# Performance work log

Hardware: AMD Instinct MI355X
Metric: run time of the kernel (lower is better)

Reference implementation:

```python
import jax, jax.numpy as jnp
import numpy as np

N, DIM, DK, DV = 8192, 512, 128, 128


def setup_inputs() -> dict:
    key = jax.random.key(0)
    ks = jax.random.split(key, 6)
    s = lambda d: 1.0 / np.sqrt(d)
    return {
        "x": jax.random.normal(ks[0], (N, DIM), jnp.float32),
        "W": jax.random.normal(ks[1], (DK, DIM), jnp.float32) * s(DIM),
        "b": jax.random.normal(ks[2], (DK,), jnp.float32) * s(DIM),
        "Wv": jax.random.normal(ks[3], (DV, DIM), jnp.float32) * s(DIM),
        "bv": jax.random.normal(ks[4], (DV,), jnp.float32) * s(DIM),
        "a": jax.random.normal(ks[5], (2 * DK,), jnp.float32),
    }


def reference(x, W, b, Wv, bv, a):
    dk = a.shape[0] // 2
    wx = x @ W.T + b                      # [n, dk]
    # additive GAT score decomposed into two matvecs + outer sum
    s_src = wx @ a[:dk]                   # [n]
    s_dst = wx @ a[dk:]                   # [n]
    score = s_src[:, None] + s_dst[None, :]  # [n, n]
    score = jax.nn.leaky_relu(score, negative_slope=0.01)
    score = jax.nn.softmax(score, axis=-1)
    v = x @ Wv.T + bv                     # [n, dv]
    return score @ v                      # [n, dv]
```

## Files before the change

### kernel.cpp

```cpp
#include <hip/hip_runtime.h>
#include <math.h>

static constexpr int N    = 8192;
static constexpr int DIM  = 512;
static constexpr int DK   = 128;
static constexpr int DV   = 128;
static constexpr float SLOPE = 0.01f;

static constexpr int NCH  = 256;
static constexpr int CHSZ = 32;
static constexpr int NCOL = 258;

static constexpr int MT  = 128;
static constexpr int BK  = 32;
static constexpr int LDT = 132;

__global__ __launch_bounds__(256) void k_front(const float* __restrict__ x,
                                               const float* __restrict__ W,
                                               const float* __restrict__ b,
                                               const float* __restrict__ a,
                                               float* __restrict__ s_src,
                                               float* __restrict__ s_dst) {
    __shared__ float sa[2 * DK];
    __shared__ float sus[DIM + 32], sud[DIM + 32];
    __shared__ float sc[2];
    int tid = threadIdx.x;
    sa[tid] = a[tid];
    __syncthreads();

    {
        float p = 0.0f;
        if (tid < 64)        p = b[tid] * sa[tid] + b[tid + 64] * sa[tid + 64];
        else if (tid < 128) { int l = tid - 64; p = b[l] * sa[DK + l] + b[l + 64] * sa[DK + 64 + l]; }
#pragma unroll
        for (int off = 32; off > 0; off >>= 1) p += __shfl_down(p, off);
        if (tid == 0)  sc[0] = p;
        if (tid == 64) sc[1] = p;
    }

#pragma unroll
    for (int half = 0; half < 2; ++half) {
        int d = tid + half * 256;
        float us = 0.0f, ud = 0.0f;
#pragma unroll 4
        for (int k = 0; k < DK; ++k) {
            float w = W[(size_t)k * DIM + d];
            us += w * sa[k];
            ud += w * sa[DK + k];
        }
        int dp = d + (d >> 6) * 4;
        sus[dp] = us;
        sud[dp] = ud;
    }
    __syncthreads();

    int r   = tid >> 3;
    int seg = tid & 7;
    int row = blockIdx.x * 32 + r;
    const float* xr = x + (size_t)row * DIM;
    int base  = seg * 64;
    int baseP = base + seg * 4;
    float accs = 0.0f, accd = 0.0f;
#pragma unroll
    for (int i = 0; i < 16; ++i) {
        float4 q  = *reinterpret_cast<const float4*>(xr + base + i * 4);
        float4 u4 = *reinterpret_cast<const float4*>(&sus[baseP + i * 4]);
        float4 w4 = *reinterpret_cast<const float4*>(&sud[baseP + i * 4]);
        accs += q.x * u4.x + q.y * u4.y + q.z * u4.z + q.w * u4.w;
        accd += q.x * w4.x + q.y * w4.y + q.z * w4.z + q.w * w4.w;
    }
#pragma unroll
    for (int off = 4; off > 0; off >>= 1) {
        accs += __shfl_down(accs, off);
        accd += __shfl_down(accd, off);
    }
    if (seg == 0) {
        s_src[row] = accs + sc[0];
        s_dst[row] = accd + sc[1];
    }
}

__global__ __launch_bounds__(256) void k_v(const float* __restrict__ x,
                                           const float* __restrict__ Wv,
                                           float* __restrict__ vpart, int ksplit) {
    __shared__ float At[BK][LDT];
    __shared__ float Bt[BK][LDT];
    int tid = threadIdx.x;
    int mt  = blockIdx.x & 63;
    int ks  = blockIdx.x >> 6;
    int row0 = mt * MT;
    int ksub = DIM / ksplit;
    int kb0  = ks * ksub;
    int nt   = ksub / BK;
    int tx = tid & 15, ty = tid >> 4;

    float acc[8][8];
#pragma unroll
    for (int i = 0; i < 8; ++i)
#pragma unroll
        for (int j = 0; j < 8; ++j) acc[i][j] = 0.0f;

    int fr[4], fk[4];
#pragma unroll
    for (int i = 0; i < 4; ++i) {
        int f = tid + i * 256;
        fr[i] = f >> 3;
        fk[i] = (f & 7) * 4;
    }
    float4 px[4], pw[4];
#pragma unroll
    for (int i = 0; i < 4; ++i) {
        px[i] = *reinterpret_cast<const float4*>(x  + (size_t)(row0 + fr[i]) * DIM + kb0 + fk[i]);
        pw[i] = *reinterpret_cast<const float4*>(Wv + (size_t)fr[i] * DIM + kb0 + fk[i]);
    }

    for (int t = 0; t < nt; ++t) {
#pragma unroll
        for (int i = 0; i < 4; ++i) {
            At[fk[i] + 0][fr[i]] = px[i].x;
            At[fk[i] + 1][fr[i]] = px[i].y;
            At[fk[i] + 2][fr[i]] = px[i].z;
            At[fk[i] + 3][fr[i]] = px[i].w;
            Bt[fk[i] + 0][fr[i]] = pw[i].x;
            Bt[fk[i] + 1][fr[i]] = pw[i].y;
            Bt[fk[i] + 2][fr[i]] = pw[i].z;
            Bt[fk[i] + 3][fr[i]] = pw[i].w;
        }
        __syncthreads();
        if (t < nt - 1) {
            int kb = kb0 + (t + 1) * BK;
#pragma unroll
            for (int i = 0; i < 4; ++i) {
                px[i] = *reinterpret_cast<const float4*>(x  + (size_t)(row0 + fr[i]) * DIM + kb + fk[i]);
                pw[i] = *reinterpret_cast<const float4*>(Wv + (size_t)fr[i] * DIM + kb + fk[i]);
            }
        }
#pragma unroll 4
        for (int kk = 0; kk < BK; ++kk) {
            float4 a0 = *reinterpret_cast<const float4*>(&At[kk][ty * 4]);
            float4 a1 = *reinterpret_cast<const float4*>(&At[kk][64 + ty * 4]);
            float4 b0 = *reinterpret_cast<const float4*>(&Bt[kk][tx * 4]);
            float4 b1 = *reinterpret_cast<const float4*>(&Bt[kk][64 + tx * 4]);
            float av[8] = {a0.x, a0.y, a0.z, a0.w, a1.x, a1.y, a1.z, a1.w};
            float bw[8] = {b0.x, b0.y, b0.z, b0.w, b1.x, b1.y, b1.z, b1.w};
#pragma unroll
            for (int i = 0; i < 8; ++i)
#pragma unroll
                for (int j = 0; j < 8; ++j) acc[i][j] += av[i] * bw[j];
        }
        __syncthreads();
    }

#pragma unroll
    for (int rh = 0; rh < 2; ++rh)
#pragma unroll
        for (int i = 0; i < 4; ++i) {
            int row = row0 + rh * 64 + ty * 4 + i;
            float* dst = vpart + ((size_t)ks * N + row) * DV;
#pragma unroll
            for (int ch = 0; ch < 2; ++ch) {
                float4 o;
                o.x = acc[rh * 4 + i][ch * 4 + 0];
                o.y = acc[rh * 4 + i][ch * 4 + 1];
                o.z = acc[rh * 4 + i][ch * 4 + 2];
                o.w = acc[rh * 4 + i][ch * 4 + 3];
                *reinterpret_cast<float4*>(dst + ch * 64 + tx * 4) = o;
            }
        }
}

__global__ void k_vred(const float* __restrict__ vpart, const float* __restrict__ bv,
                       float* __restrict__ v, int ksplit) {
    int fi = blockIdx.x * 256 + threadIdx.x;
    const float4* vp = reinterpret_cast<const float4*>(vpart);
    float4 s = vp[fi];
    for (int ksp = 1; ksp < ksplit; ++ksp) {
        float4 q = vp[(size_t)ksp * (N * DV / 4) + fi];
        s.x += q.x; s.y += q.y; s.z += q.z; s.w += q.w;
    }
    float4 bb = reinterpret_cast<const float4*>(bv)[fi & 31];
    s.x += bb.x; s.y += bb.y; s.z += bb.z; s.w += bb.w;
    reinterpret_cast<float4*>(v)[fi] = s;
}

__global__ __launch_bounds__(256) void k_rank_scatter(const float* __restrict__ s_dst,
                                                      float* __restrict__ d_sorted,
                                                      int* __restrict__ perm) {
    __shared__ __align__(16) float sd[N];
    __shared__ int part[256];
    int tid = threadIdx.x;
    for (int t = tid; t < N / 4; t += 256)
        reinterpret_cast<float4*>(sd)[t] = reinterpret_cast<const float4*>(s_dst)[t];
    __syncthreads();
    int j0  = blockIdx.x * 16;
    int jj  = tid >> 4;
    int seg = tid & 15;
    int j   = j0 + jj;
    float dj = sd[j];
    int cnt = 0;
    const float4* sdv = reinterpret_cast<const float4*>(sd);
    int cbase = seg * 128;
    for (int c = 0; c < 128; ++c) {
        float4 q = sdv[cbase + c];
        int i0 = (cbase + c) * 4;
        cnt += (q.x < dj || (q.x == dj && (i0 + 0) < j));
        cnt += (q.y < dj || (q.y == dj && (i0 + 1) < j));
        cnt += (q.z < dj || (q.z == dj && (i0 + 2) < j));
        cnt += (q.w < dj || (q.w == dj && (i0 + 3) < j));
    }
    part[tid] = cnt;
    __syncthreads();
    if (tid < 16) {
        int s = 0;
#pragma unroll
        for (int t = 0; t < 16; ++t) s += part[tid * 16 + t];
        int jw = j0 + tid;
        d_sorted[s] = sd[jw];
        perm[s] = jw;
    }
}

__global__ void k_chunk_tot(const float* __restrict__ d_sorted, const int* __restrict__ perm,
                            const float* __restrict__ v, double* __restrict__ chunk_tot) {
    int ch = blockIdx.x, tid = threadIdx.x;
    __shared__ float e1s[CHSZ], e2s[CHSZ];
    __shared__ int pk[CHSZ];
    float dmax = d_sorted[N - 1];
    if (tid < CHSZ) {
        float d = d_sorted[ch * CHSZ + tid];
        e1s[tid] = expf(d - dmax);
        e2s[tid] = expf(SLOPE * d);
        pk[tid]  = perm[ch * CHSZ + tid];
    }
    __syncthreads();
    int col = tid & 127;
    bool isP2 = tid >= 128;
    double acc = 0.0;
    for (int k = 0; k < CHSZ; ++k) {
        float e = isP2 ? e2s[k] : e1s[k];
        acc += (double)e * (double)v[(size_t)pk[k] * DV + col];
    }
    chunk_tot[(size_t)ch * NCOL + tid] = acc;
    if (tid == 0) {
        double z = 0.0;
        for (int k = 0; k < CHSZ; ++k) z += (double)e1s[k];
        chunk_tot[(size_t)ch * NCOL + 256] = z;
    }
    if (tid == 1) {
        double z = 0.0;
        for (int k = 0; k < CHSZ; ++k) z += (double)e2s[k];
        chunk_tot[(size_t)ch * NCOL + 257] = z;
    }
}

__global__ void k_chunk_off(const double* __restrict__ chunk_tot, double* __restrict__ chunk_off,
                            double* __restrict__ totals) {
    __shared__ double s[256];
    int col = blockIdx.x;
    int tid = threadIdx.x;
    double val = chunk_tot[(size_t)tid * NCOL + col];
    s[tid] = val;
    __syncthreads();
    for (int off = 1; off < 256; off <<= 1) {
        double t = (tid >= off) ? s[tid - off] : 0.0;
        __syncthreads();
        s[tid] += t;
        __syncthreads();
    }
    chunk_off[(size_t)tid * NCOL + col] = s[tid] - val;
    if (tid == 255) totals[col] = s[255];
}

__global__ void k_scan(const float* __restrict__ d_sorted, const int* __restrict__ perm,
                       const float* __restrict__ v, const double* __restrict__ chunk_off,
                       float* __restrict__ P1, float* __restrict__ P2,
                       double* __restrict__ pz1, double* __restrict__ pz2) {
    int ch = blockIdx.x, tid = threadIdx.x;
    __shared__ float e1s[CHSZ], e2s[CHSZ];
    __shared__ int pk[CHSZ];
    float dmax = d_sorted[N - 1];
    if (tid < CHSZ) {
        float d = d_sorted[ch * CHSZ + tid];
        e1s[tid] = expf(d - dmax);
        e2s[tid] = expf(SLOPE * d);
        pk[tid]  = perm[ch * CHSZ + tid];
    }
    __syncthreads();
    int col = tid & 127;
    bool isP2 = tid >= 128;
    float* P = isP2 ? P2 : P1;
    double acc = chunk_off[(size_t)ch * NCOL + tid];
    for (int k = 0; k < CHSZ; ++k) {
        int kg = ch * CHSZ + k;
        P[(size_t)kg * DV + col] = (float)acc;
        float e = isP2 ? e2s[k] : e1s[k];
        acc += (double)e * (double)v[(size_t)pk[k] * DV + col];
    }
    if (tid == 0) {
        double z = chunk_off[(size_t)ch * NCOL + 256];
        for (int k = 0; k < CHSZ; ++k) { pz1[ch * CHSZ + k] = z; z += (double)e1s[k]; }
    }
    if (tid == 1) {
        double z = chunk_off[(size_t)ch * NCOL + 257];
        for (int k = 0; k < CHSZ; ++k) { pz2[ch * CHSZ + k] = z; z += (double)e2s[k]; }
    }
}

__global__ __launch_bounds__(256) void k_final(const float* __restrict__ s_src,
                                               const float* __restrict__ d_sorted,
                                               const float* __restrict__ P1,
                                               const float* __restrict__ P2,
                                               const double* __restrict__ pz1,
                                               const double* __restrict__ pz2,
                                               const double* __restrict__ totals,
                                               float* __restrict__ out) {
    __shared__ int ski[8];
    __shared__ float ssi[8];
    int tid = threadIdx.x;
    int rbase = blockIdx.x * 8;
    if (tid < 8) {
        int row = rbase + tid;
        float si = s_src[row];
        float thr = -si;
        int lo = 0, hi = N;
        while (lo < hi) {
            int mid = (lo + hi) >> 1;
            if (d_sorted[mid] <= thr) lo = mid + 1; else hi = mid;
        }
        ski[tid] = lo;
        ssi[tid] = si;
    }
    __syncthreads();
    float dmax = d_sorted[N - 1];
    int dv = tid & 127;
    int half = tid >> 7;
    double T1 = totals[dv];
    double T2 = totals[128 + dv];
    double z1T = totals[256], z2T = totals[257];
#pragma unroll
    for (int it = 0; it < 4; ++it) {
        int r2 = it * 2 + half;
        int row = rbase + r2;
        float si = ssi[r2];
        int ki = ski[r2];
        float t = si + dmax;
        float m = t > 0.0f ? t : SLOPE * t;
        float alpha = expf(t - m);
        float beta  = expf(SLOPE * si - m);
        double suf1, sufz1, pre2, prez2;
        if (ki < N) {
            suf1  = T1 - (double)P1[(size_t)ki * DV + dv];
            sufz1 = z1T - pz1[ki];
            pre2  = (double)P2[(size_t)ki * DV + dv];
            prez2 = pz2[ki];
        } else {
            suf1 = 0.0; sufz1 = 0.0; pre2 = T2; prez2 = z2T;
        }
        double num = (double)alpha * suf1  + (double)beta * pre2;
        double den = (double)alpha * sufz1 + (double)beta * prez2;
        out[(size_t)row * DV + dv] = (float)(num / den);
    }
}

extern "C" void kernel_launch(void* const* d_in, const int* in_sizes, int n_in,
                              void* d_out, int out_size, void* d_ws, size_t ws_size,
                              hipStream_t stream) {
    const float* x  = (const float*)d_in[0];
    const float* W  = (const float*)d_in[1];
    const float* b  = (const float*)d_in[2];
    const float* Wv = (const float*)d_in[3];
    const float* bv = (const float*)d_in[4];
    const float* a  = (const float*)d_in[5];
    float* out = (float*)d_out;

    char* base = (char*)d_ws;
    size_t off = 0;
    auto carve = [&](size_t bytes) -> void* {
        void* p = base + off;
        off = (off + bytes + 255) & ~(size_t)255;
        return p;
    };
    float*  s_src     = (float*)carve(N * sizeof(float));
    float*  s_dst     = (float*)carve(N * sizeof(float));
    float*  d_sorted  = (float*)carve(N * sizeof(float));
    int*    perm      = (int*)carve(N * sizeof(int));
    double* pz1       = (double*)carve(N * sizeof(double));
    double* pz2       = (double*)carve(N * sizeof(double));
    double* chunk_tot = (double*)carve((size_t)NCH * NCOL * sizeof(double));
    double* chunk_off = (double*)carve((size_t)NCH * NCOL * sizeof(double));
    double* totals    = (double*)carve(NCOL * sizeof(double));

    const size_t planeB = (size_t)N * DV * sizeof(float);
    size_t avail = ws_size > off ? ws_size - off : 0;
    int ksplit = 2;
    if (avail >= 8 * planeB + 4096)      ksplit = 8;
    else if (avail >= 4 * planeB + 4096) ksplit = 4;
    size_t unionBytes = (size_t)(ksplit > 2 ? ksplit : 2) * planeB;
    char* uni = (char*)carve(unionBytes);
    float* vpart = (float*)uni;
    float* P1    = (float*)uni;
    float* P2    = (float*)(uni + planeB);
    float* v     = out;

    k_front<<<N / 32, 256, 0, stream>>>(x, W, b, a, s_src, s_dst);
    k_v<<<64 * ksplit, 256, 0, stream>>>(x, Wv, vpart, ksplit);
    k_vred<<<N * DV / 4 / 256, 256, 0, stream>>>(vpart, bv, v, ksplit);
    k_rank_scatter<<<N / 16, 256, 0, stream>>>(s_dst, d_sorted, perm);
    k_chunk_tot<<<NCH, 256, 0, stream>>>(d_sorted, perm, v, chunk_tot);
    k_chunk_off<<<NCOL, 256, 0, stream>>>(chunk_tot, chunk_off, totals);
    k_scan<<<NCH, 256, 0, stream>>>(d_sorted, perm, v, chunk_off, P1, P2, pz1, pz2);
    k_final<<<N / 8, 256, 0, stream>>>(s_src, d_sorted, P1, P2, pz1, pz2, totals, out);
}
```

Baseline: 169.3 us.

## Fuse V split-K reduction into chunk totals and precompute weighted sorted rows

Removes the separate V reduction kernel. The partial sums are now reduced directly in the chunk-total kernel, which gathers rows through the sort permutation and writes exp-weighted, sorted Y1/Y2 planes. The scan kernel then streams contiguous Y rows instead of doing permuted gathers and recomputing the weights. Chunk size is halved to 16 with 512 chunks, and the offset scan now folds chunk pairs per thread. The cost is two extra N×DV fp32 buffers written and read back, plus float rather than double products in the chunk totals.

```diff
diff --git a/kernel.cpp b/kernel.cpp
--- a/kernel.cpp
+++ b/kernel.cpp
@@ -7,8 +7,8 @@
 static constexpr int DV   = 128;
 static constexpr float SLOPE = 0.01f;
 
-static constexpr int NCH  = 256;
-static constexpr int CHSZ = 32;
+static constexpr int NCH  = 512;
+static constexpr int CHSZ = 16;
 static constexpr int NCOL = 258;
 
 static constexpr int MT  = 128;
@@ -167,20 +167,6 @@
                 *reinterpret_cast<float4*>(dst + ch * 64 + tx * 4) = o;
             }
         }
-}
-
-__global__ void k_vred(const float* __restrict__ vpart, const float* __restrict__ bv,
-                       float* __restrict__ v, int ksplit) {
-    int fi = blockIdx.x * 256 + threadIdx.x;
-    const float4* vp = reinterpret_cast<const float4*>(vpart);
-    float4 s = vp[fi];
-    for (int ksp = 1; ksp < ksplit; ++ksp) {
-        float4 q = vp[(size_t)ksp * (N * DV / 4) + fi];
-        s.x += q.x; s.y += q.y; s.z += q.z; s.w += q.w;
-    }
-    float4 bb = reinterpret_cast<const float4*>(bv)[fi & 31];
-    s.x += bb.x; s.y += bb.y; s.z += bb.z; s.w += bb.w;
-    reinterpret_cast<float4*>(v)[fi] = s;
 }
 
 __global__ __launch_bounds__(256) void k_rank_scatter(const float* __restrict__ s_dst,
@@ -220,89 +206,126 @@
     }
 }
 
-__global__ void k_chunk_tot(const float* __restrict__ d_sorted, const int* __restrict__ perm,
-                            const float* __restrict__ v, double* __restrict__ chunk_tot) {
-    int ch = blockIdx.x, tid = threadIdx.x;
-    __shared__ float e1s[CHSZ], e2s[CHSZ];
-    __shared__ int pk[CHSZ];
+__global__ __launch_bounds__(256) void k_vredY(const float* __restrict__ vpart,
+                                               const float* __restrict__ bv,
+                                               const float* __restrict__ d_sorted,
+                                               const int* __restrict__ perm,
+                                               float* __restrict__ Y1,
+                                               float* __restrict__ Y2,
+                                               double* __restrict__ chunk_tot,
+                                               int ksplit) {
+    __shared__ float sv[CHSZ][DV];
+    __shared__ float se1[CHSZ], se2[CHSZ];
+    int ch  = blockIdx.x;
+    int tid = threadIdx.x;
+    int g   = tid >> 5;
+    int c4  = tid & 31;
     float dmax = d_sorted[N - 1];
     if (tid < CHSZ) {
         float d = d_sorted[ch * CHSZ + tid];
-        e1s[tid] = expf(d - dmax);
-        e2s[tid] = expf(SLOPE * d);
-        pk[tid]  = perm[ch * CHSZ + tid];
+        se1[tid] = expf(d - dmax);
+        se2[tid] = expf(SLOPE * d);
+    }
+    __syncthreads();
+    float4 bb = reinterpret_cast<const float4*>(bv)[c4];
+#pragma unroll
+    for (int half = 0; half < 2; ++half) {
+        int rl = half * 8 + g;
+        int r  = ch * CHSZ + rl;
+        int j  = perm[r];
+        float4 s = {0.f, 0.f, 0.f, 0.f};
+        for (int ksp = 0; ksp < ksplit; ++ksp) {
+            float4 q = *reinterpret_cast<const float4*>(vpart + ((size_t)ksp * N + j) * DV + c4 * 4);
+            s.x += q.x; s.y += q.y; s.z += q.z; s.w += q.w;
+        }
+        s.x += bb.x; s.y += bb.y; s.z += bb.z; s.w += bb.w;
+        *reinterpret_cast<float4*>(&sv[rl][c4 * 4]) = s;
+        float e1 = se1[rl], e2 = se2[rl];
+        float4 o1 = {e1 * s.x, e1 * s.y, e1 * s.z, e1 * s.w};
+        float4 o2 = {e2 * s.x, e2 * s.y, e2 * s.z, e2 * s.w};
+        *reinterpret_cast<float4*>(Y1 + (size_t)r * DV + c4 * 4) = o1;
+        *reinterpret_cast<float4*>(Y2 + (size_t)r * DV + c4 * 4) = o2;
     }
     __syncthreads();
     int col = tid & 127;
-    bool isP2 = tid >= 128;
+    bool is2 = tid >= 128;
     double acc = 0.0;
+#pragma unroll
     for (int k = 0; k < CHSZ; ++k) {
-        float e = isP2 ? e2s[k] : e1s[k];
-        acc += (double)e * (double)v[(size_t)pk[k] * DV + col];
+        float e = is2 ? se2[k] : se1[k];
+        acc += (double)(e * sv[k][col]);
     }
     chunk_tot[(size_t)ch * NCOL + tid] = acc;
     if (tid == 0) {
         double z = 0.0;
-        for (int k = 0; k < CHSZ; ++k) z += (double)e1s[k];
+#pragma unroll
+        for (int k = 0; k < CHSZ; ++k) z += (double)se1[k];
         chunk_tot[(size_t)ch * NCOL + 256] = z;
     }
     if (tid == 1) {
         double z = 0.0;
-        for (int k = 0; k < CHSZ; ++k) z += (double)e2s[k];
+#pragma unroll
+        for (int k = 0; k < CHSZ; ++k) z += (double)se2[k];
         chunk_tot[(size_t)ch * NCOL + 257] = z;
     }
 }
 
-__global__ void k_chunk_off(const double* __restrict__ chunk_tot, double* __restrict__ chunk_off,
-                            double* __restrict__ totals) {
-    __shared__ double s[256];
+__global__ __launch_bounds__(256) void k_coff(const double* __restrict__ chunk_tot,
+                                              double* __restrict__ chunk_off,
+                                              double* __restrict__ totals) {
+    __shared__ double sp[256];
     int col = blockIdx.x;
     int tid = threadIdx.x;
-    double val = chunk_tot[(size_t)tid * NCOL + col];
-    s[tid] = val;
+    double v0 = chunk_tot[(size_t)(2 * tid) * NCOL + col];
+    double v1 = chunk_tot[(size_t)(2 * tid + 1) * NCOL + col];
+    double p = v0 + v1;
+    sp[tid] = p;
     __syncthreads();
     for (int off = 1; off < 256; off <<= 1) {
-        double t = (tid >= off) ? s[tid - off] : 0.0;
+        double t = (tid >= off) ? sp[tid - off] : 0.0;
         __syncthreads();
-        s[tid] += t;
+        sp[tid] += t;
         __syncthreads();
     }
-    chunk_off[(size_t)tid * NCOL + col] = s[tid] - val;
-    if (tid == 255) totals[col] = s[255];
-}
-
-__global__ void k_scan(const float* __restrict__ d_sorted, const int* __restrict__ perm,
-                       const float* __restrict__ v, const double* __restrict__ chunk_off,
-                       float* __restrict__ P1, float* __restrict__ P2,
-                       double* __restrict__ pz1, double* __restrict__ pz2) {
-    int ch = blockIdx.x, tid = threadIdx.x;
-    __shared__ float e1s[CHSZ], e2s[CHSZ];
-    __shared__ int pk[CHSZ];
-    float dmax = d_sorted[N - 1];
-    if (tid < CHSZ) {
-        float d = d_sorted[ch * CHSZ + tid];
-        e1s[tid] = expf(d - dmax);
-        e2s[tid] = expf(SLOPE * d);
-        pk[tid]  = perm[ch * CHSZ + tid];
-    }
-    __syncthreads();
+    double excl = sp[tid] - p;
+    chunk_off[(size_t)(2 * tid) * NCOL + col]     = excl;
+    chunk_off[(size_t)(2 * tid + 1) * NCOL + col] = excl + v0;
+    if (tid == 255) totals[col] = sp[255];
+}
+
+__global__ __launch_bounds__(256) void k_scanW(const float* __restrict__ Y1,
+                                               const float* __restrict__ Y2,
+                                               const float* __restrict__ d_sorted,
+                                               const double* __restrict__ chunk_off,
+                                               float* __restrict__ P1,
+                                               float* __restrict__ P2,
+                                               double* __restrict__ pz1,
+                                               double* __restrict__ pz2) {
+    int ch  = blockIdx.x;
+    int tid = threadIdx.x;
     int col = tid & 127;
-    bool isP2 = tid >= 128;
-    float* P = isP2 ? P2 : P1;
+    bool is2 = tid >= 128;
+    const float* Y = is2 ? Y2 : Y1;
+    float* P       = is2 ? P2 : P1;
     double acc = chunk_off[(size_t)ch * NCOL + tid];
+#pragma unroll
     for (int k = 0; k < CHSZ; ++k) {
-        int kg = ch * CHSZ + k;
-        P[(size_t)kg * DV + col] = (float)acc;
-        float e = isP2 ? e2s[k] : e1s[k];
-        acc += (double)e * (double)v[(size_t)pk[k] * DV + col];
-    }
-    if (tid == 0) {
-        double z = chunk_off[(size_t)ch * NCOL + 256];
-        for (int k = 0; k < CHSZ; ++k) { pz1[ch * CHSZ + k] = z; z += (double)e1s[k]; }
-    }
-    if (tid == 1) {
-        double z = chunk_off[(size_t)ch * NCOL + 257];
-        for (int k = 0; k < CHSZ; ++k) { pz2[ch * CHSZ + k] = z; z += (double)e2s[k]; }
+        size_t idx = (size_t)(ch * CHSZ + k) * DV + col;
+        P[idx] = (float)acc;
+        acc += (double)Y[idx];
+    }
+    if (tid < 2) {
+        float dmax = d_sorted[N - 1];
+        double z = chunk_off[(size_t)ch * NCOL + 256 + tid];
+        double* pz = tid == 0 ? pz1 : pz2;
+#pragma unroll
+        for (int k = 0; k < CHSZ; ++k) {
+            int r = ch * CHSZ + k;
+            float d = d_sorted[r];
+            float e = (tid == 0) ? expf(d - dmax) : expf(SLOPE * d);
+            pz[r] = z;
+            z += (double)e;
+        }
     }
 }
 
@@ -389,6 +412,8 @@
     double* chunk_tot = (double*)carve((size_t)NCH * NCOL * sizeof(double));
     double* chunk_off = (double*)carve((size_t)NCH * NCOL * sizeof(double));
     double* totals    = (double*)carve(NCOL * sizeof(double));
+    float*  Y1        = (float*)carve((size_t)N * DV * sizeof(float));
+    float*  Y2        = (float*)carve((size_t)N * DV * sizeof(float));
 
     const size_t planeB = (size_t)N * DV * sizeof(float);
     size_t avail = ws_size > off ? ws_size - off : 0;
@@ -400,14 +425,12 @@
     float* vpart = (float*)uni;
     float* P1    = (float*)uni;
     float* P2    = (float*)(uni + planeB);
-    float* v     = out;
 
     k_front<<<N / 32, 256, 0, stream>>>(x, W, b, a, s_src, s_dst);
     k_v<<<64 * ksplit, 256, 0, stream>>>(x, Wv, vpart, ksplit);
-    k_vred<<<N * DV / 4 / 256, 256, 0, stream>>>(vpart, bv, v, ksplit);
     k_rank_scatter<<<N / 16, 256, 0, stream>>>(s_dst, d_sorted, perm);
-    k_chunk_tot<<<NCH, 256, 0, stream>>>(d_sorted, perm, v, chunk_tot);
-    k_chunk_off<<<NCOL, 256, 0, stream>>>(chunk_tot, chunk_off, totals);
-    k_scan<<<NCH, 256, 0, stream>>>(d_sorted, perm, v, chunk_off, P1, P2, pz1, pz2);
+    k_vredY<<<NCH, 256, 0, stream>>>(vpart, bv, d_sorted, perm, Y1, Y2, chunk_tot, ksplit);
+    k_coff<<<NCOL, 256, 0, stream>>>(chunk_tot, chunk_off, totals);
+    k_scanW<<<NCH, 256, 0, stream>>>(Y1, Y2, d_sorted, chunk_off, P1, P2, pz1, pz2);
     k_final<<<N / 8, 256, 0, stream>>>(s_src, d_sorted, P1, P2, pz1, pz2, totals, out);
 }
```

Result: no change. 169.1 us (-0.1%).
